# Kernel tuning notes

Measured on AMD Instinct MI355X. Metric: run time of the kernel, lower is better.

The kernel has to match this reference:

```python
import jax, jax.numpy as jnp
import numpy as np

B, T, V, H, L = 32, 128, 50257, 1024, 2


def setup_inputs() -> dict:
    key = jax.random.key(0)
    ks = jax.random.split(key, 8)
    s_in = 0.02   # small init to keep gates unsaturated
    return {
        "tokens": jax.random.randint(ks[0], (B, T), 0, V, dtype=jnp.int32),
        "embedding": jax.random.normal(ks[1], (V, H), jnp.float32) * s_in,
        "W_ih": jax.random.normal(ks[2], (L, 4 * H, H), jnp.float32) * s_in,
        "W_hh": jax.random.normal(ks[3], (L, 4 * H, H), jnp.float32) * s_in,
        "b_ih": jax.random.normal(ks[4], (L, 4 * H), jnp.float32) * s_in,
        "b_hh": jax.random.normal(ks[5], (L, 4 * H), jnp.float32) * s_in,
        "W_out": jax.random.normal(ks[6], (V, H), jnp.float32) * s_in,
        "b_out": jax.random.normal(ks[7], (V,), jnp.float32) * s_in,
        "h0": jnp.zeros((L, B, H), jnp.float32),
        "c0": jnp.zeros((L, B, H), jnp.float32),
    }


def reference(tokens, embedding, W_ih, W_hh, b_ih, b_hh, W_out, b_out, h0, c0):
    # Teacher-forced LSTM LM: embed -> L-layer LSTM (PyTorch gate order i,f,g,o)
    # -> vocab projection -> log-softmax. Dropout is identity (p=0 / eval).
    x = embedding[tokens]                      # [B,T,H]
    xs = jnp.swapaxes(x, 0, 1)                 # [T,B,H] time-major for scan
    n_layers = W_ih.shape[0]

    def step(carry, x_t):
        h, c = carry                           # each [L,B,H]
        inp = x_t
        hs, cs = [], []
        for l in range(n_layers):
            gates = inp @ W_ih[l].T + b_ih[l] + h[l] @ W_hh[l].T + b_hh[l]  # [B,4H]
            i_g, f_g, g_g, o_g = jnp.split(gates, 4, axis=-1)
            i_g = jax.nn.sigmoid(i_g)
            f_g = jax.nn.sigmoid(f_g)
            g_g = jnp.tanh(g_g)
            o_g = jax.nn.sigmoid(o_g)
            c_new = f_g * c[l] + i_g * g_g
            h_new = o_g * jnp.tanh(c_new)
            hs.append(h_new)
            cs.append(c_new)
            inp = h_new
        return (jnp.stack(hs), jnp.stack(cs)), inp

    (hT, cT), outs = jax.lax.scan(step, (h0, c0), xs)   # outs: [T,B,H]
    outs = jnp.swapaxes(outs, 0, 1)                     # [B,T,H]
    logits = outs @ W_out.T + b_out                     # [B,T,V]
    logp = jax.nn.log_softmax(logits, axis=-1)
    return logp, hT, cT
```

## Files before the change

kernel.cpp:

```cpp
#include <hip/hip_runtime.h>
#include <hip/hip_bf16.h>
#include <cstdint>
#include <cstddef>

#define DEVI __device__ __forceinline__

typedef __attribute__((ext_vector_type(8))) short short8;
typedef __attribute__((ext_vector_type(4))) float f32x4;
using u16 = unsigned short;

constexpr int BSZ = 32, TSZ = 128, VSZ = 50257, HSZ = 1024;
constexpr int M4 = BSZ * TSZ;
constexpr int FH = 4 * HSZ;
constexpr long long OUT_LOGP = (long long)M4 * VSZ;
constexpr int NWRK = 192;
constexpr int NBLK = 256;
constexpr int LDSB = 147584;
constexpr int LDBF = 50258;
constexpr int NNT = 393;
constexpr int CVT_PER = 12;
constexpr int CVTILES = 64 * CVT_PER;

DEVI u16 f2bf(float f) {
  unsigned u = __float_as_uint(f);
  unsigned r = (u + 0x7fffu + ((u >> 16) & 1u)) >> 16;
  return (u16)r;
}
DEVI u16 f2bf_hw(float f) {
  __hip_bfloat16 h = __float2bfloat16(f);
  return __builtin_bit_cast(u16, h);
}
DEVI float bf2f(u16 u) { return __uint_as_float(((unsigned)u) << 16); }
DEVI float sigm(float x) { return 1.f / (1.f + __expf(-x)); }
DEVI float tanh_fast(float x) { return 1.f - 2.f / (1.f + __expf(2.f * x)); }

DEVI f32x4 mfma16(short8 a, short8 b, f32x4 c) {
  return __builtin_amdgcn_mfma_f32_16x16x32_bf16(a, b, c, 0, 0, 0);
}

DEVI void gld16(const void* g, void* l) {
  auto gp = (const __attribute__((address_space(1))) unsigned int*)g;
  auto lp = (__attribute__((address_space(3))) unsigned int*)l;
  __builtin_amdgcn_global_load_lds(gp, lp, 16, 0, 0);
}

DEVI void cohld16x16(const u16* base, short8 (&d)[16]) {
  asm volatile(
      "global_load_dwordx4 %0, %16, off sc0 sc1\n\t"
      "global_load_dwordx4 %1, %16, off offset:64 sc0 sc1\n\t"
      "global_load_dwordx4 %2, %16, off offset:128 sc0 sc1\n\t"
      "global_load_dwordx4 %3, %16, off offset:192 sc0 sc1\n\t"
      "global_load_dwordx4 %4, %16, off offset:256 sc0 sc1\n\t"
      "global_load_dwordx4 %5, %16, off offset:320 sc0 sc1\n\t"
      "global_load_dwordx4 %6, %16, off offset:384 sc0 sc1\n\t"
      "global_load_dwordx4 %7, %16, off offset:448 sc0 sc1\n\t"
      "global_load_dwordx4 %8, %16, off offset:512 sc0 sc1\n\t"
      "global_load_dwordx4 %9, %16, off offset:576 sc0 sc1\n\t"
      "global_load_dwordx4 %10, %16, off offset:640 sc0 sc1\n\t"
      "global_load_dwordx4 %11, %16, off offset:704 sc0 sc1\n\t"
      "global_load_dwordx4 %12, %16, off offset:768 sc0 sc1\n\t"
      "global_load_dwordx4 %13, %16, off offset:832 sc0 sc1\n\t"
      "global_load_dwordx4 %14, %16, off offset:896 sc0 sc1\n\t"
      "global_load_dwordx4 %15, %16, off offset:960 sc0 sc1\n\t"
      "s_waitcnt vmcnt(0)"
      : "=&v"(d[0]), "=&v"(d[1]), "=&v"(d[2]), "=&v"(d[3]),
        "=&v"(d[4]), "=&v"(d[5]), "=&v"(d[6]), "=&v"(d[7]),
        "=&v"(d[8]), "=&v"(d[9]), "=&v"(d[10]), "=&v"(d[11]),
        "=&v"(d[12]), "=&v"(d[13]), "=&v"(d[14]), "=&v"(d[15])
      : "v"(base)
      : "memory");
}
DEVI void cohst2_u16(u16* p0, u16 v0, u16* p1, u16 v1) {
  asm volatile(
      "global_store_short %0, %2, off sc0 sc1\n\t"
      "global_store_short %1, %3, off sc0 sc1\n\t"
      "s_waitcnt vmcnt(0)"
      :: "v"(p0), "v"(p1), "v"((unsigned)v0), "v"((unsigned)v1)
      : "memory");
}
DEVI void cohst1_u16(u16* p0, u16 v0) {
  asm volatile(
      "global_store_short %0, %1, off sc0 sc1\n\t"
      "s_waitcnt vmcnt(0)"
      :: "v"(p0), "v"((unsigned)v0)
      : "memory");
}
DEVI void flagst(unsigned* p, unsigned v) {
  __hip_atomic_store(p, v, __ATOMIC_RELAXED, __HIP_MEMORY_SCOPE_AGENT);
}
DEVI unsigned flagld(const unsigned* p) {
  return __hip_atomic_load(p, __ATOMIC_RELAXED, __HIP_MEMORY_SCOPE_AGENT);
}

DEVI void wait64(const unsigned* f, unsigned g, int l) {
  while (!__all((int)(flagld(f + l) >= g))) __builtin_amdgcn_s_sleep(1);
}
DEVI void wait128(const unsigned* f, unsigned g, int l) {
  for (;;) {
    unsigned a = flagld(f + l);
    unsigned b = flagld(f + 64 + l);
    if (__all((int)((a >= g) && (b >= g)))) break;
    __builtin_amdgcn_s_sleep(1);
  }
}

__global__ void prep_all(const float* __restrict__ bih, const float* __restrict__ bhh,
                         float* __restrict__ bias0, float* __restrict__ rowsum,
                         unsigned* __restrict__ bar, const float* __restrict__ h0,
                         u16* __restrict__ H0, u16* __restrict__ h1init) {
  int i = blockIdx.x * 256 + threadIdx.x;
  H0[i] = f2bf(h0[i]);
  h1init[i] = f2bf(h0[BSZ * HSZ + i]);
  if (i < FH) { bias0[i] = bih[i] + bhh[i]; rowsum[i] = 0.f; }
  if (i < 1024) bar[i] = 0u;
}

__global__ void cvt_bf16(const float* __restrict__ src, u16* __restrict__ dst, int n4) {
  int i = blockIdx.x * blockDim.x + threadIdx.x;
  int stride = gridDim.x * blockDim.x;
  for (; i < n4; i += stride) {
    float4 v = ((const float4*)src)[i];
    ushort4 o; o.x = f2bf(v.x); o.y = f2bf(v.y); o.z = f2bf(v.z); o.w = f2bf(v.w);
    ((ushort4*)dst)[i] = o;
  }
}

__global__ __launch_bounds__(256) void embed_kernel(const int* __restrict__ tok,
                                                    const float* __restrict__ emb,
                                                    u16* __restrict__ X) {
  int m = blockIdx.x;
  int t = m >> 5, b = m & 31;
  int token = tok[b * TSZ + t];
  const float4* src = (const float4*)(emb + (size_t)token * HSZ);
  int i = threadIdx.x;
  float4 v = src[i];
  ushort4 o; o.x = f2bf(v.x); o.y = f2bf(v.y); o.z = f2bf(v.z); o.w = f2bf(v.w);
  *(ushort4*)(X + (size_t)m * HSZ + i * 4) = o;
}

template <int EPI, bool BCVT, bool TMAJ>
DEVI void gemm_tile(char* smemg, const u16* __restrict__ A, const void* __restrict__ Bsrc,
                    void* __restrict__ Cout, const float* __restrict__ bias,
                    float* __restrict__ rowsum, int m0, int n0, int N, int K, int ldc) {
  u16* As = (u16*)smemg;
  u16* Bs = (u16*)(smemg + 16384);
  float* epi = (float*)smemg;
  const int tid = threadIdx.x;
  const int l = tid & 63, wid = tid >> 6;
  const int wm = wid >> 1, wn = wid & 1;

  const int srow8 = tid >> 3;
  const int scol = ((tid & 7) * 8) ^ ((srow8 & 7) << 3);
  u16* AsW = As + (size_t)(tid >> 6) * 8 * 64;
  u16* BsW = Bs + (size_t)(tid >> 6) * 8 * 64;

  const u16* Bbf = (const u16*)Bsrc;
  const float* Bf32 = (const float*)Bsrc;

  f32x4 acc[4][4];
  f32x4 z = {0.f, 0.f, 0.f, 0.f};
#pragma unroll
  for (int a = 0; a < 4; ++a)
#pragma unroll
    for (int b = 0; b < 4; ++b) acc[a][b] = z;

  for (int k0 = 0; k0 < K; k0 += 64) {
#pragma unroll
    for (int rr = 0; rr < 4; ++rr) {
      gld16(A + (size_t)(m0 + rr * 32 + srow8) * K + k0 + scol, AsW + rr * 2048);
      if (!BCVT) {
        int br = n0 + rr * 32 + srow8; if (br > N - 1) br = N - 1;
        gld16(Bbf + (size_t)br * K + k0 + scol, BsW + rr * 2048);
      }
    }
    if (BCVT) {
#pragma unroll
      for (int half = 0; half < 2; ++half) {
        const int row = half * 64 + (tid >> 2);
        int br = n0 + row; if (br > N - 1) br = N - 1;
        const int c0 = (tid & 3) * 16;
        const float* s = Bf32 + (size_t)br * K + k0 + c0;
        const int sw = (row & 7) << 3;
        float4 x0 = *(const float4*)s,       y0 = *(const float4*)(s + 4);
        float4 x1 = *(const float4*)(s + 8), y1 = *(const float4*)(s + 12);
        short8 v0, v1;
        v0[0]=(short)f2bf(x0.x); v0[1]=(short)f2bf(x0.y); v0[2]=(short)f2bf(x0.z); v0[3]=(short)f2bf(x0.w);
        v0[4]=(short)f2bf(y0.x); v0[5]=(short)f2bf(y0.y); v0[6]=(short)f2bf(y0.z); v0[7]=(short)f2bf(y0.w);
        v1[0]=(short)f2bf(x1.x); v1[1]=(short)f2bf(x1.y); v1[2]=(short)f2bf(x1.z); v1[3]=(short)f2bf(x1.w);
        v1[4]=(short)f2bf(y1.x); v1[5]=(short)f2bf(y1.y); v1[6]=(short)f2bf(y1.z); v1[7]=(short)f2bf(y1.w);
        *(short8*)&Bs[row * 64 + (c0 ^ sw)] = v0;
        *(short8*)&Bs[row * 64 + ((c0 + 8) ^ sw)] = v1;
      }
    }
    __syncthreads();
#pragma unroll
    for (int ks = 0; ks < 2; ++ks) {
      short8 af[4], bfr[4];
#pragma unroll
      for (int x = 0; x < 4; ++x) {
        const int ar = wm * 64 + x * 16 + (l & 15);
        const int ka = (ks * 64 + (l >> 4) * 16) ^ ((ar & 7) << 4);
        af[x] = *(const short8*)((const char*)As + ar * 128 + ka);
        const int br = wn * 64 + x * 16 + (l & 15);
        const int kb = (ks * 64 + (l >> 4) * 16) ^ ((br & 7) << 4);
        bfr[x] = *(const short8*)((const char*)Bs + br * 128 + kb);
      }
#pragma unroll
      for (int mf = 0; mf < 4; ++mf)
#pragma unroll
        for (int nf = 0; nf < 4; ++nf)
          acc[mf][nf] = mfma16(af[mf], bfr[nf], acc[mf][nf]);
    }
    __syncthreads();
  }

  if constexpr (EPI == 2) {
    u16* C = (u16*)Cout;
#pragma unroll
    for (int mf = 0; mf < 4; ++mf) {
      int rbase = m0 + wm * 64 + mf * 16 + ((l >> 4) << 2);
      float bvr[4];
#pragma unroll
      for (int j = 0; j < 4; ++j) bvr[j] = bias[rbase + j];
#pragma unroll
      for (int nf = 0; nf < 4; ++nf) {
        int cg = n0 + wn * 64 + nf * 16 + (l & 15);
#pragma unroll
        for (int j = 0; j < 4; ++j)
          C[(size_t)(rbase + j) * ldc + cg] = f2bf_hw(acc[mf][nf][j] + bvr[j]);
      }
    }
  } else if constexpr (EPI == 3) {
    u16* C = (u16*)Cout;
    float* ep = epi + wid * 1024;
    const int lq4 = l >> 4, l15e = l & 15;
    float bv[4];
#pragma unroll
    for (int nf = 0; nf < 4; ++nf) {
      int cg = n0 + wn * 64 + nf * 16 + l15e;
      bv[nf] = (cg < N) ? bias[cg] : 0.f;
    }
    const int r8 = l >> 3, c8 = l & 7;
    const int colb8 = n0 + wn * 64 + c8 * 8;
#pragma unroll
    for (int mf = 0; mf < 4; ++mf) {
#pragma unroll
      for (int nf = 0; nf < 4; ++nf)
#pragma unroll
        for (int j = 0; j < 4; ++j)
          ep[(lq4 * 4 + j) * 64 + nf * 16 + l15e] = acc[mf][nf][j] + bv[nf];
      asm volatile("s_waitcnt lgkmcnt(0)" ::: "memory");
      __builtin_amdgcn_sched_barrier(0);
#pragma unroll
      for (int pass = 0; pass < 2; ++pass) {
        const int rr = pass * 8 + r8;
        f32x4 v0 = *(const f32x4*)&ep[rr * 64 + c8 * 8];
        f32x4 v1 = *(const f32x4*)&ep[rr * 64 + c8 * 8 + 4];
        const int row = m0 + wm * 64 + mf * 16 + rr;
        const int orow = TMAJ ? ((row & 31) * TSZ + (row >> 5)) : row;
        float e = 0.f;
        if (colb8 + 7 < N) {
          short8 o;
          o[0]=(short)f2bf_hw(v0[0]); o[1]=(short)f2bf_hw(v0[1]);
          o[2]=(short)f2bf_hw(v0[2]); o[3]=(short)f2bf_hw(v0[3]);
          o[4]=(short)f2bf_hw(v1[0]); o[5]=(short)f2bf_hw(v1[1]);
          o[6]=(short)f2bf_hw(v1[2]); o[7]=(short)f2bf_hw(v1[3]);
          *(short8*)&C[(size_t)orow * ldc + colb8] = o;
          e = __expf(v0[0]) + __expf(v0[1]) + __expf(v0[2]) + __expf(v0[3]) +
              __expf(v1[0]) + __expf(v1[1]) + __expf(v1[2]) + __expf(v1[3]);
        } else {
#pragma unroll
          for (int kk = 0; kk < 8; ++kk) {
            float fv = (kk < 4) ? v0[kk] : v1[kk - 4];
            if (colb8 + kk < N) {
              C[(size_t)orow * ldc + colb8 + kk] = f2bf_hw(fv);
              e += __expf(fv);
            }
          }
        }
        e += __shfl_xor(e, 1, 8); e += __shfl_xor(e, 2, 8); e += __shfl_xor(e, 4, 8);
        if (c8 == 0) atomicAdd(&rowsum[orow], e);
      }
      asm volatile("s_waitcnt lgkmcnt(0)" ::: "memory");
      __builtin_amdgcn_sched_barrier(0);
    }
  } else {
    float* C = (float*)Cout;
    float* ep = epi + wid * 1024;
    const int lq4 = l >> 4, l15e = l & 15;
    float bv[4];
#pragma unroll
    for (int nf = 0; nf < 4; ++nf) {
      int cg = n0 + wn * 64 + nf * 16 + l15e;
      bv[nf] = (cg < N) ? bias[cg] : 0.f;
    }
    const int colbase = n0 + wn * 64 + l15e * 4;
#pragma unroll
    for (int mf = 0; mf < 4; ++mf) {
#pragma unroll
      for (int nf = 0; nf < 4; ++nf)
#pragma unroll
        for (int j = 0; j < 4; ++j)
          ep[(lq4 * 4 + j) * 64 + nf * 16 + l15e] = acc[mf][nf][j] + bv[nf];
      asm volatile("s_waitcnt lgkmcnt(0)" ::: "memory");
      __builtin_amdgcn_sched_barrier(0);
#pragma unroll
      for (int pass = 0; pass < 4; ++pass) {
        const int rr = pass * 4 + lq4;
        f32x4 v = *(const f32x4*)&ep[rr * 64 + l15e * 4];
        const int row = m0 + wm * 64 + mf * 16 + rr;
        const int orow = TMAJ ? ((row & 31) * TSZ + (row >> 5)) : row;
        float e = 0.f;
        if (colbase + 3 < N) {
          *(f32x4*)&C[(size_t)orow * ldc + colbase] = v;
          e = __expf(v[0]) + __expf(v[1]) + __expf(v[2]) + __expf(v[3]);
        } else {
#pragma unroll
          for (int kk = 0; kk < 4; ++kk)
            if (colbase + kk < N) {
              C[(size_t)orow * ldc + colbase + kk] = v[kk];
              e += __expf(v[kk]);
            }
        }
        e += __shfl_xor(e, 1, 16); e += __shfl_xor(e, 2, 16);
        e += __shfl_xor(e, 4, 16); e += __shfl_xor(e, 8, 16);
        if (l15e == 0) atomicAdd(&rowsum[orow], e);
      }
      asm volatile("s_waitcnt lgkmcnt(0)" ::: "memory");
      __builtin_amdgcn_sched_barrier(0);
    }
  }
}

template <int EPI, bool BCVT, int MAP, bool TMAJ>
__global__ __launch_bounds__(256) void gemm_bt(const u16* __restrict__ A,
                                               const void* __restrict__ Bsrc,
                                               void* __restrict__ Cout,
                                               const float* __restrict__ bias,
                                               float* __restrict__ rowsum,
                                               int nm, int nn, int N, int K, int ldc,
                                               int wofs) {
  __shared__ char smemg[32768];
  const int id = blockIdx.x;
  int bm, bn;
  if constexpr (MAP == 2) {
    const int gsz = (int)gridDim.x;
    int wg = ((gsz & 7) == 0) ? (id % 8) * (gsz >> 3) + (id >> 3) : id;
    int w = wofs + wg;
    bm = w / nn; bn = w % nn;
  } else {
    const int gsz = nm * nn;
    int wg = ((gsz & 7) == 0) ? (id % 8) * (gsz >> 3) + (id >> 3) : id;
    bm = wg % nm; bn = wg / nm;
  }
  gemm_tile<EPI, BCVT, TMAJ>(smemg, A, Bsrc, Cout, bias, rowsum,
                             bm * 128, bn * 128, N, K, ldc);
}

struct LstmArgs {
  const u16* G0T;
  const float* Wih;
  const float* Whh;
  const float* bih, *bhh, *c0;
  u16* H0;
  u16* H1;
  const u16* h1init;
  float* out_hc;
  unsigned* bar;
  const float* Wout;
  u16* Woutbf;
  u16* Lbf;
  const float* bout;
  float* rowsum;
  int mode;
};

DEVI void stage_row_q(const float* src, char* row, int sw, int q) {
  for (int kk = 0; kk < 256; kk += 8) {
    float4 x = *(const float4*)(src + kk);
    float4 y = *(const float4*)(src + kk + 4);
    short8 v;
    v[0]=(short)f2bf(x.x); v[1]=(short)f2bf(x.y); v[2]=(short)f2bf(x.z); v[3]=(short)f2bf(x.w);
    v[4]=(short)f2bf(y.x); v[5]=(short)f2bf(y.y); v[6]=(short)f2bf(y.z); v[7]=(short)f2bf(y.w);
    const int kbyte = (q * 256 + kk) * 2;
    *(short8*)(row + (kbyte ^ sw)) = v;
  }
}

DEVI short8 ldsB(const char* lds, int r, int kbyte) {
  return *(const short8*)(lds + (size_t)r * 2048 + (kbyte ^ ((r & 7) << 4)));
}

DEVI void part_wr(float* part, int wstride_log2, int wv, int R, int lq, f32x4 v) {
  *(f32x4*)&part[(wv << wstride_log2) + (R << 4) + ((lq ^ (R & 3)) << 2)] = v;
}
DEVI float part_rd(const float* part, int wstride_log2, int wv, int R, int c) {
  return part[(wv << wstride_log2) + (R << 4) + ((((c >> 2) ^ (R & 3)) << 2)) + (c & 3)];
}

__global__ __launch_bounds__(256, 1) void lstm_coop(LstmArgs A) {
  extern __shared__ char smem[];
  const int wg = blockIdx.x, tid = threadIdx.x;
  const int wv = tid >> 6, l = tid & 63;
  const int l15 = l & 15, lq = l >> 4;
  const int bh = wv >> 1, kh = wv & 1;

  if (wg < 64) {
    char* WL = smem;
    float* part = (float*)(smem + 131072);
    const int j0 = wg << 4;
    {
      const int R = tid >> 2, q = tid & 3;
      const int grow = ((R >> 4) << 10) + j0 + (R & 15);
      stage_row_q(A.Whh + (size_t)grow * HSZ + q * 256, WL + (size_t)R * 2048,
                  (R & 7) << 4, q);
    }
    const int uu = tid & 15, bb = tid >> 4;
    float cst[2];
    cst[0] = A.c0[(size_t)bb * HSZ + j0 + uu];
    cst[1] = A.c0[(size_t)(bb + 16) * HSZ + j0 + uu];
    __syncthreads();
    unsigned* myflag = A.bar + wg;

    for (int t = 0; t < TSZ; ++t) {
      float g0v[4][2];
      {
        const int col = t * 32;
#pragma unroll
        for (int g4 = 0; g4 < 4; ++g4) {
          const u16* gp = A.G0T + (size_t)((g4 << 10) + j0 + uu) * M4 + col;
          g0v[g4][0] = bf2f(gp[bb]);
          g0v[g4][1] = bf2f(gp[bb + 16]);
        }
      }
      if (t > 0) wait64(A.bar, (unsigned)t, l);
      const u16* hprev = A.H0 + (size_t)t * (BSZ * HSZ);
      const u16* hb = hprev + (size_t)(bh * 16 + l15) * HSZ + (kh << 9) + (lq << 3);
      short8 a[16];
      cohld16x16(hb, a);
      __builtin_amdgcn_sched_barrier(0);
      f32x4 acc[4];
      { f32x4 z = {0.f,0.f,0.f,0.f}; acc[0]=z; acc[1]=z; acc[2]=z; acc[3]=z; }
#pragma unroll
      for (int k = 0; k < 16; ++k) {
        const int kbyte = (((kh << 4) + k) << 6) + (lq << 4);
#pragma unroll
        for (int tr = 0; tr < 4; ++tr)
          acc[tr] = mfma16(a[k], ldsB(WL, (tr << 4) + l15, kbyte), acc[tr]);
      }
#pragma unroll
      for (int tr = 0; tr < 4; ++tr)
        part_wr(part, 10, wv, (tr << 4) + l15, lq, acc[tr]);
      __syncthreads();
      const bool last = (t == TSZ - 1);
      u16* hnext = A.H0 + (size_t)(t + 1) * (BSZ * HSZ);
      u16 hv[2];
#pragma unroll
      for (int pp = 0; pp < 2; ++pp) {
        const int b = bb + (pp << 4);
        float gi = g0v[0][pp], gf = g0v[1][pp], gg = g0v[2][pp], go = g0v[3][pp];
#pragma unroll
        for (int kh2 = 0; kh2 < 2; ++kh2) {
          const int w2 = (pp << 1) | kh2;
          gi += part_rd(part, 10, w2, uu, bb);
          gf += part_rd(part, 10, w2, 16 + uu, bb);
          gg += part_rd(part, 10, w2, 32 + uu, bb);
          go += part_rd(part, 10, w2, 48 + uu, bb);
        }
        float i_ = sigm(gi), f_ = sigm(gf), g_ = tanh_fast(gg), o_ = sigm(go);
        float c_ = f_ * cst[pp] + i_ * g_;
        cst[pp] = c_;
        float h_ = o_ * tanh_fast(c_);
        hv[pp] = f2bf(h_);
        if (last) {
          A.out_hc[(size_t)b * HSZ + j0 + uu] = h_;
          A.out_hc[2 * BSZ * HSZ + (size_t)b * HSZ + j0 + uu] = c_;
        }
      }
      cohst2_u16(hnext + (size_t)bb * HSZ + j0 + uu, hv[0],
                 hnext + (size_t)(bb + 16) * HSZ + j0 + uu, hv[1]);
      __syncthreads();
      if (tid == 0) flagst(myflag, (unsigned)(t + 1));
    }
  } else if (wg < NWRK) {
    char* WxL = smem;
    char* WhL = smem + 65536;
    float* part = (float*)(smem + 131072);
    float* biasL = (float*)(smem + 139264);
    const int lw = wg - 64;
    const int j1 = lw << 3;
    {
      const int rr = tid >> 2, q = tid & 3;
      const int r = rr & 31;
      const int grow = FH + ((r >> 3) << 10) + j1 + (r & 7);
      const float* base = (rr >= 32) ? A.Whh : A.Wih;
      char* dst = ((rr >= 32) ? WhL : WxL) + (size_t)r * 2048;
      stage_row_q(base + (size_t)grow * HSZ + q * 256, dst, (r & 7) << 4, q);
    }
    if (tid < 32) {
      const int grow = FH + ((tid >> 3) << 10) + j1 + (tid & 7);
      biasL[tid] = A.bih[grow] + A.bhh[grow];
    }
    const int uu = tid & 7, b1 = tid >> 3;
    float cst = A.c0[BSZ * HSZ + (size_t)b1 * HSZ + j1 + uu];
    __syncthreads();
    unsigned* myflag = A.bar + 64 + lw;

    for (int t = 0; t < TSZ; ++t) {
      wait64(A.bar, (unsigned)(t + 1), l);
      const u16* x1 = A.H0 + (size_t)(t + 1) * (BSZ * HSZ);
      const u16* xb = x1 + (size_t)(bh * 16 + l15) * HSZ + (kh << 9) + (lq << 3);
      short8 ax[16];
      cohld16x16(xb, ax);
      __builtin_amdgcn_sched_barrier(0);
      f32x4 acc[2];
      { f32x4 z = {0.f,0.f,0.f,0.f}; acc[0]=z; acc[1]=z; }
#pragma unroll
      for (int k = 0; k < 16; ++k) {
        const int kbyte = (((kh << 4) + k) << 6) + (lq << 4);
        acc[0] = mfma16(ax[k], ldsB(WxL, l15, kbyte), acc[0]);
        acc[1] = mfma16(ax[k], ldsB(WxL, 16 + l15, kbyte), acc[1]);
      }
      if (t > 0) wait128(A.bar + 64, (unsigned)t, l);
      const u16* hp = (t == 0) ? A.h1init : A.H1 + (size_t)(t - 1) * (BSZ * HSZ);
      const u16* hbp = hp + (size_t)(bh * 16 + l15) * HSZ + (kh << 9) + (lq << 3);
      short8 ah[16];
      cohld16x16(hbp, ah);
      __builtin_amdgcn_sched_barrier(0);
#pragma unroll
      for (int k = 0; k < 16; ++k) {
        const int kbyte = (((kh << 4) + k) << 6) + (lq << 4);
        acc[0] = mfma16(ah[k], ldsB(WhL, l15, kbyte), acc[0]);
        acc[1] = mfma16(ah[k], ldsB(WhL, 16 + l15, kbyte), acc[1]);
      }
#pragma unroll
      for (int tr = 0; tr < 2; ++tr)
        part_wr(part, 9, wv, (tr << 4) + l15, lq, acc[tr]);
      __syncthreads();
      const bool last = (t == TSZ - 1);
      {
        const int c = b1 & 15, ph = b1 >> 4;
        float gi = biasL[uu], gf = biasL[8 + uu], gg = biasL[16 + uu], go = biasL[24 + uu];
#pragma unroll
        for (int kh2 = 0; kh2 < 2; ++kh2) {
          const int w2 = (ph << 1) | kh2;
          gi += part_rd(part, 9, w2, uu, c);
          gf += part_rd(part, 9, w2, 8 + uu, c);
          gg += part_rd(part, 9, w2, 16 + uu, c);
          go += part_rd(part, 9, w2, 24 + uu, c);
        }
        float i_ = sigm(gi), f_ = sigm(gf), g_ = tanh_fast(gg), o_ = sigm(go);
        float c_ = f_ * cst + i_ * g_;
        cst = c_;
        float h_ = o_ * tanh_fast(c_);
        cohst1_u16(A.H1 + (size_t)t * (BSZ * HSZ) + (size_t)b1 * HSZ + j1 + uu, f2bf(h_));
        if (last) {
          A.out_hc[BSZ * HSZ + (size_t)b1 * HSZ + j1 + uu] = h_;
          A.out_hc[3 * BSZ * HSZ + (size_t)b1 * HSZ + j1 + uu] = c_;
        }
      }
      __syncthreads();
      if (tid == 0) flagst(myflag, (unsigned)(t + 1));
    }
  } else {
    const int cid = wg - NWRK;
    if (A.mode >= 1) {
      const int n4 = (int)((size_t)VSZ * HSZ / 4);
      const float4* src = (const float4*)A.Wout;
      ushort4* dst = (ushort4*)A.Woutbf;
      for (int i = cid * 256 + tid; i < n4; i += 64 * 256) {
        float4 v = src[i];
        ushort4 o;
        o.x = f2bf_hw(v.x); o.y = f2bf_hw(v.y); o.z = f2bf_hw(v.z); o.w = f2bf_hw(v.w);
        dst[i] = o;
      }
      asm volatile("s_waitcnt vmcnt(0)" ::: "memory");
      __builtin_amdgcn_fence(__ATOMIC_RELEASE, "agent");
      __syncthreads();
      if (tid == 0) flagst(A.bar + 192 + cid, 1u);
      if (A.mode == 2) {
        wait64(A.bar + 192, 1u, l);
        __syncthreads();
        for (int k = 0; k < CVT_PER; ++k) {
          const int w = cid + (k << 6);
          const int bm = w / NNT, bn = w % NNT;
          wait128(A.bar + 64, (unsigned)(4 * bm + 4), l);
          __syncthreads();
          gemm_tile<3, false, true>(smem, A.H1, A.Woutbf, A.Lbf, A.bout, A.rowsum,
                                    bm * 128, bn * 128, VSZ, HSZ, LDBF);
        }
      }
    }
  }
}

__global__ void lse_kernel(float* __restrict__ rowsum, int n) {
  int i = blockIdx.x * 256 + threadIdx.x;
  if (i < n) rowsum[i] = logf(rowsum[i]);
}

__global__ __launch_bounds__(256) void lsm_finish(float* __restrict__ C,
                                                  const float* __restrict__ lse, int Vd) {
  int row = blockIdx.y;
  size_t start = (size_t)row * (size_t)Vd;
  float s = lse[row];
  int i = blockIdx.x * 256 + threadIdx.x;
  int col = i * 4;
  if (col + 3 < Vd) {
    f32x4* p = (f32x4*)(C + start + col);
    f32x4 v = *p;
    v[0] -= s; v[1] -= s; v[2] -= s; v[3] -= s;
    *p = v;
  } else {
    for (int j = col; j < Vd; ++j) C[start + j] -= s;
  }
}

__global__ __launch_bounds__(256) void lsm_finish_bf(const u16* __restrict__ L,
                                                     float* __restrict__ out,
                                                     const float* __restrict__ rowsum,
                                                     int Vd, int ldl) {
  int row = blockIdx.y;
  float s = logf(rowsum[row]);
  int col = blockIdx.x * 2048 + threadIdx.x * 8;
  const u16* lp = L + (size_t)row * ldl;
  float* op = out + (size_t)row * Vd;
  if (col + 7 < Vd) {
    short8 v = *(const short8*)(lp + col);
    f32x4 a, b;
    a[0] = bf2f((u16)v[0]) - s; a[1] = bf2f((u16)v[1]) - s;
    a[2] = bf2f((u16)v[2]) - s; a[3] = bf2f((u16)v[3]) - s;
    b[0] = bf2f((u16)v[4]) - s; b[1] = bf2f((u16)v[5]) - s;
    b[2] = bf2f((u16)v[6]) - s; b[3] = bf2f((u16)v[7]) - s;
    *(f32x4*)(op + col) = a;
    *(f32x4*)(op + col + 4) = b;
  } else {
    for (int j = col; j < Vd; ++j) op[j] = bf2f(lp[j]) - s;
  }
}

extern "C" void kernel_launch(void* const* d_in, const int* in_sizes, int n_in,
                              void* d_out, int out_size, void* d_ws, size_t ws_size,
                              hipStream_t stream) {
  const int* tokens = (const int*)d_in[0];
  const float* emb = (const float*)d_in[1];
  const float* Wih = (const float*)d_in[2];
  const float* Whh = (const float*)d_in[3];
  const float* bih = (const float*)d_in[4];
  const float* bhh = (const float*)d_in[5];
  const float* Wout = (const float*)d_in[6];
  const float* bout = (const float*)d_in[7];
  const float* h0 = (const float*)d_in[8];
  const float* c0 = (const float*)d_in[9];
  float* out = (float*)d_out;

  char* w = (char*)d_ws;
  size_t o = 0;
  u16* Xbf = (u16*)(w + o);    o += (size_t)M4 * HSZ * 2;
  u16* Wih0bf = (u16*)(w + o); o += (size_t)FH * HSZ * 2;
  u16* G0T = (u16*)(w + o);    o += (size_t)FH * M4 * 2;
  u16* H0 = (u16*)(w + o);     o += (size_t)(TSZ + 1) * BSZ * HSZ * 2;
  u16* H1 = (u16*)(w + o);     o += (size_t)BSZ * TSZ * HSZ * 2;
  u16* h1init = (u16*)(w + o); o += (size_t)BSZ * HSZ * 2;
  float* bias0 = (float*)(w + o);  o += FH * 4;
  float* rowsum = (float*)(w + o); o += M4 * 4;
  unsigned* bar = (unsigned*)(w + o); o += 4096;
  u16* Woutbf = (u16*)(w + o);
  size_t need_full = o + (size_t)VSZ * HSZ * 2;
  u16* Lbf = (u16*)(w + need_full);
  size_t need_lbf = need_full + (size_t)M4 * LDBF * 2;
  const bool bcvt = (ws_size < need_full);
  const bool bf16c = (ws_size >= need_lbf);
  const int mode = bcvt ? 0 : (bf16c ? 2 : 1);

  prep_all<<<128, 256, 0, stream>>>(bih, bhh, bias0, rowsum, bar, h0, H0, h1init);
  cvt_bf16<<<2048, 256, 0, stream>>>(Wih, Wih0bf, FH * HSZ / 4);
  embed_kernel<<<M4, 256, 0, stream>>>(tokens, emb, Xbf);
  gemm_bt<2, false, 0, false><<<32 * 32, 256, 0, stream>>>(
      Wih0bf, Xbf, G0T, bias0, nullptr, 32, 32, M4, HSZ, M4, 0);

  LstmArgs la{G0T, Wih, Whh, bih, bhh, c0, H0, H1, h1init,
              out + (size_t)OUT_LOGP, bar, Wout, Woutbf, Lbf, bout, rowsum, mode};
  void* kargs[] = {&la};
  hipFuncSetAttribute((const void*)lstm_coop, hipFuncAttributeMaxDynamicSharedMemorySize, LDSB);
  hipLaunchCooperativeKernel((const void*)lstm_coop, dim3(NBLK), dim3(256), kargs, LDSB, stream);

  const int TOT = 32 * NNT;
  if (bf16c) {
    gemm_bt<3, false, 2, true><<<TOT - CVTILES, 256, 0, stream>>>(
        H1, Woutbf, Lbf, bout, rowsum, 32, NNT, VSZ, HSZ, LDBF, CVTILES);
    lsm_finish_bf<<<dim3(25, M4), 256, 0, stream>>>(Lbf, out, rowsum, VSZ, LDBF);
  } else if (!bcvt) {
    gemm_bt<1, false, 2, true><<<TOT, 256, 0, stream>>>(
        H1, Woutbf, out, bout, rowsum, 32, NNT, VSZ, HSZ, VSZ, 0);
    lse_kernel<<<16, 256, 0, stream>>>(rowsum, M4);
    lsm_finish<<<dim3((VSZ + 1023) / 1024, M4), 256, 0, stream>>>(out, rowsum, VSZ);
  } else {
    gemm_bt<1, true, 2, true><<<TOT, 256, 0, stream>>>(
        H1, Wout, out, bout, rowsum, 32, NNT, VSZ, HSZ, VSZ, 0);
    lse_kernel<<<16, 256, 0, stream>>>(rowsum, M4);
    lsm_finish<<<dim3((VSZ + 1023) / 1024, M4), 256, 0, stream>>>(out, rowsum, VSZ);
  }
}
```

Measured before the change: 1.663 ms.

## Fuse vocab projection and log-softmax finish with per-row-block completion counters

Replaces the separate projection GEMM and log-softmax finish kernels with one kernel. GEMM blocks bump a per-row-block atomic counter when they finish, and trailing finisher blocks spin on that counter and then write the fp32 log-probabilities for that row block. This lets the finish pass overlap the remaining GEMM tiles and removes a launch. The LSTM kernel's in-kernel projection tiles are widened to two full row blocks so those rows can be finished early. The risk is spinning finisher blocks taking compute slots and depending on block dispatch order to avoid deadlock.

```diff
diff --git a/kernel.cpp b/kernel.cpp
--- a/kernel.cpp
+++ b/kernel.cpp
@@ -18,8 +18,9 @@
 constexpr int LDSB = 147584;
 constexpr int LDBF = 50258;
 constexpr int NNT = 393;
-constexpr int CVT_PER = 12;
-constexpr int CVTILES = 64 * CVT_PER;
+constexpr int CVTILES = 786;
+constexpr int PROJ_IDS = 12576;
+constexpr int NFIN = 512;
 
 DEVI u16 f2bf(float f) {
   unsigned u = __float_as_uint(f);
@@ -85,6 +86,12 @@
       :: "v"(p0), "v"((unsigned)v0)
       : "memory");
 }
+DEVI float cohld_f32(const float* p) {
+  unsigned r;
+  asm volatile("global_load_dword %0, %1, off sc0 sc1\n\ts_waitcnt vmcnt(0)"
+               : "=v"(r) : "v"(p) : "memory");
+  return __uint_as_float(r);
+}
 DEVI void flagst(unsigned* p, unsigned v) {
   __hip_atomic_store(p, v, __ATOMIC_RELAXED, __HIP_MEMORY_SCOPE_AGENT);
 }
@@ -357,6 +364,65 @@
                              bm * 128, bn * 128, N, K, ldc);
 }
 
+__global__ __launch_bounds__(256) void proj_fused(const u16* __restrict__ H1,
+                                                  const u16* __restrict__ Woutbf,
+                                                  u16* __restrict__ Lbf,
+                                                  const float* __restrict__ bout,
+                                                  float* __restrict__ rowsum,
+                                                  float* __restrict__ out,
+                                                  unsigned* __restrict__ cnt) {
+  __shared__ char smemg[32768];
+  const int id = blockIdx.x;
+  if (id < PROJ_IDS) {
+    const int g = id & 7, p = id >> 3;
+    int bm, bn;
+    if (g < 6) {
+      bm = 2 + g * 4 + p / NNT; bn = p % NNT;
+    } else {
+      if (p >= 3 * NNT) return;
+      bm = 26 + (g - 6) * 3 + p / NNT; bn = p % NNT;
+    }
+    gemm_tile<3, false, true>(smemg, H1, Woutbf, Lbf, bout, rowsum,
+                              bm * 128, bn * 128, VSZ, HSZ, LDBF);
+    asm volatile("s_waitcnt vmcnt(0)" ::: "memory");
+    __builtin_amdgcn_fence(__ATOMIC_RELEASE, "agent");
+    __syncthreads();
+    if (threadIdx.x == 0)
+      __hip_atomic_fetch_add(cnt + bm, 1u, __ATOMIC_RELEASE, __HIP_MEMORY_SCOPE_AGENT);
+  } else {
+    const int f = id - PROJ_IDS;
+    const int bm = (f < 32) ? (f >> 4) : (2 + ((f - 32) >> 4));
+    const int fi = (f < 32) ? (f & 15) : ((f - 32) & 15);
+    if (threadIdx.x == 0) {
+      while (__hip_atomic_load(cnt + bm, __ATOMIC_ACQUIRE, __HIP_MEMORY_SCOPE_AGENT) < (unsigned)NNT)
+        __builtin_amdgcn_s_sleep(4);
+    }
+    __syncthreads();
+    __builtin_amdgcn_fence(__ATOMIC_ACQUIRE, "agent");
+    for (int j = fi * 8; j < fi * 8 + 8; ++j) {
+      const int r = bm * 128 + j;
+      const int orow = ((r & 31) << 7) + (r >> 5);
+      const float s = logf(cohld_f32(rowsum + orow));
+      const u16* lp = Lbf + (size_t)orow * LDBF;
+      float* op = out + (size_t)orow * VSZ;
+      for (int col = (int)threadIdx.x * 8; col < VSZ; col += 2048) {
+        if (col + 7 < VSZ) {
+          short8 v = *(const short8*)(lp + col);
+          f32x4 a, b;
+          a[0] = bf2f((u16)v[0]) - s; a[1] = bf2f((u16)v[1]) - s;
+          a[2] = bf2f((u16)v[2]) - s; a[3] = bf2f((u16)v[3]) - s;
+          b[0] = bf2f((u16)v[4]) - s; b[1] = bf2f((u16)v[5]) - s;
+          b[2] = bf2f((u16)v[6]) - s; b[3] = bf2f((u16)v[7]) - s;
+          *(f32x4*)(op + col) = a;
+          *(f32x4*)(op + col + 4) = b;
+        } else {
+          for (int k = col; k < VSZ; ++k) op[k] = bf2f(lp[k]) - s;
+        }
+      }
+    }
+  }
+}
+
 struct LstmArgs {
   const u16* G0T;
   const float* Wih;
@@ -581,13 +647,18 @@
       if (A.mode == 2) {
         wait64(A.bar + 192, 1u, l);
         __syncthreads();
-        for (int k = 0; k < CVT_PER; ++k) {
-          const int w = cid + (k << 6);
+        unsigned* cnt = A.bar + 256;
+        for (int w = cid; w < CVTILES; w += 64) {
           const int bm = w / NNT, bn = w % NNT;
           wait128(A.bar + 64, (unsigned)(4 * bm + 4), l);
           __syncthreads();
           gemm_tile<3, false, true>(smem, A.H1, A.Woutbf, A.Lbf, A.bout, A.rowsum,
                                     bm * 128, bn * 128, VSZ, HSZ, LDBF);
+          asm volatile("s_waitcnt vmcnt(0)" ::: "memory");
+          __builtin_amdgcn_fence(__ATOMIC_RELEASE, "agent");
+          __syncthreads();
+          if (tid == 0)
+            __hip_atomic_fetch_add(cnt + bm, 1u, __ATOMIC_RELEASE, __HIP_MEMORY_SCOPE_AGENT);
         }
       }
     }
@@ -613,29 +684,6 @@
     *p = v;
   } else {
     for (int j = col; j < Vd; ++j) C[start + j] -= s;
-  }
-}
-
-__global__ __launch_bounds__(256) void lsm_finish_bf(const u16* __restrict__ L,
-                                                     float* __restrict__ out,
-                                                     const float* __restrict__ rowsum,
-                                                     int Vd, int ldl) {
-  int row = blockIdx.y;
-  float s = logf(rowsum[row]);
-  int col = blockIdx.x * 2048 + threadIdx.x * 8;
-  const u16* lp = L + (size_t)row * ldl;
-  float* op = out + (size_t)row * Vd;
-  if (col + 7 < Vd) {
-    short8 v = *(const short8*)(lp + col);
-    f32x4 a, b;
-    a[0] = bf2f((u16)v[0]) - s; a[1] = bf2f((u16)v[1]) - s;
-    a[2] = bf2f((u16)v[2]) - s; a[3] = bf2f((u16)v[3]) - s;
-    b[0] = bf2f((u16)v[4]) - s; b[1] = bf2f((u16)v[5]) - s;
-    b[2] = bf2f((u16)v[6]) - s; b[3] = bf2f((u16)v[7]) - s;
-    *(f32x4*)(op + col) = a;
-    *(f32x4*)(op + col + 4) = b;
-  } else {
-    for (int j = col; j < Vd; ++j) op[j] = bf2f(lp[j]) - s;
   }
 }
 
@@ -685,17 +733,17 @@
   hipFuncSetAttribute((const void*)lstm_coop, hipFuncAttributeMaxDynamicSharedMemorySize, LDSB);
   hipLaunchCooperativeKernel((const void*)lstm_coop, dim3(NBLK), dim3(256), kargs, LDSB, stream);
 
-  const int TOT = 32 * NNT;
   if (bf16c) {
-    gemm_bt<3, false, 2, true><<<TOT - CVTILES, 256, 0, stream>>>(
-        H1, Woutbf, Lbf, bout, rowsum, 32, NNT, VSZ, HSZ, LDBF, CVTILES);
-    lsm_finish_bf<<<dim3(25, M4), 256, 0, stream>>>(Lbf, out, rowsum, VSZ, LDBF);
+    proj_fused<<<PROJ_IDS + NFIN, 256, 0, stream>>>(H1, Woutbf, Lbf, bout, rowsum,
+                                                    out, bar + 256);
   } else if (!bcvt) {
+    const int TOT = 32 * NNT;
     gemm_bt<1, false, 2, true><<<TOT, 256, 0, stream>>>(
         H1, Woutbf, out, bout, rowsum, 32, NNT, VSZ, HSZ, VSZ, 0);
     lse_kernel<<<16, 256, 0, stream>>>(rowsum, M4);
     lsm_finish<<<dim3((VSZ + 1023) / 1024, M4), 256, 0, stream>>>(out, rowsum, VSZ);
   } else {
+    const int TOT = 32 * NNT;
     gemm_bt<1, true, 2, true><<<TOT, 256, 0, stream>>>(
         H1, Wout, out, bout, rowsum, 32, NNT, VSZ, HSZ, VSZ, 0);
     lse_kernel<<<16, 256, 0, stream>>>(rowsum, M4);
```

New measurement: 4.238 ms. 2.55x slower.
